# Optimization experiments

Hardware: AMD Instinct MI355X
Metric: run time of the kernel (lower is better)

Reference implementation:

```python
import jax, jax.numpy as jnp
import numpy as np

B, S, D = 2, 2048, 1024
N_QK, N_V, N_KNOW = 4096, 4096, 8192
N_HEADS = 16
MAX_K_QK, MAX_K_V, MAX_K_KNOW = 32, 32, 64
LN_EPS = 1e-6


def _unit_norm(key, shape, scale=1.0):
    x = jax.random.normal(key, shape, jnp.float32)
    return x / (jnp.linalg.norm(x, axis=-1, keepdims=True) + 1e-8) * scale


def setup_inputs() -> dict:
    key = jax.random.key(0)
    ks = jax.random.split(key, 12)
    return {
        "x": jax.random.normal(ks[0], (B, S, D), jnp.float32),
        "qk_emb": _unit_norm(ks[1], (N_QK, D)),
        "qk_w": _unit_norm(ks[2], (N_QK, D)),
        "v_emb": _unit_norm(ks[3], (N_V, D)),
        "v_w": _unit_norm(ks[4], (N_V, D)),
        "know_emb": _unit_norm(ks[5], (N_KNOW, D)),
        "know_w": _unit_norm(ks[6], (N_KNOW, D)),
        "tau_attn_k": jax.random.normal(ks[7], (D, 3), jnp.float32) * (1.0 / np.sqrt(D)),
        "tau_attn_b": jnp.zeros((3,), jnp.float32),
        "tau_know_k": jax.random.normal(ks[8], (D, 1), jnp.float32) * (1.0 / np.sqrt(D)),
        "tau_know_b": jnp.zeros((1,), jnp.float32),
        "expand_O": jax.random.normal(ks[9], (D, D), jnp.float32) * 0.02,
        "ln1_scale": jnp.ones((D,), jnp.float32),
        "ln1_bias": jnp.zeros((D,), jnp.float32),
        "ln2_scale": jnp.ones((D,), jnp.float32),
        "ln2_bias": jnp.zeros((D,), jnp.float32),
    }


def _layer_norm(x, scale, bias):
    mean = jnp.mean(x, axis=-1, keepdims=True)
    var = jnp.mean(jnp.square(x - mean), axis=-1, keepdims=True)
    return (x - mean) / jnp.sqrt(var + LN_EPS) * scale + bias


def threshold_gate(scores, tau, max_k):
    # scores: [B,S,N], tau: [B,S,1]
    raw = scores - tau
    gate = jnp.where(raw > 0, raw, 1e-8 * jnp.exp(raw))
    exp_gate = jnp.exp(gate) - 1.0
    topk_vals, _ = jax.lax.top_k(exp_gate, min(max_k, scores.shape[-1]))
    thr = topk_vals[:, :, -1:]
    exp_gate = jnp.where(exp_gate >= thr, exp_gate, 0.0)
    gate_sum = exp_gate.sum(axis=-1, keepdims=True) + 1e-8
    strength = jnp.tanh(exp_gate.max(axis=-1, keepdims=True))
    return exp_gate / gate_sum * strength


@jax.checkpoint
def sense_emit_full(x, emb, w, gate):
    # [B,S,D] @ [D,N] -> gated [B,S,N] -> [B,S,D]
    return ((x @ emb.T) * gate) @ w


def _block(x, qk_emb, qk_w, v_emb, v_w, know_emb, know_w,
           tau_attn_k, tau_attn_b, tau_know_k, tau_know_b,
           expand_O, ln1_scale, ln1_bias, ln2_scale, ln2_bias):
    # ---- attention circuit (deterministic; dropout = identity) ----
    normed = _layer_norm(x, ln1_scale, ln1_bias)
    scores_qk = normed @ qk_emb.T           # [B,S,N_QK]
    scores_v = normed @ v_emb.T             # [B,S,N_V]
    tau_all = normed @ tau_attn_k + tau_attn_b  # [B,S,3]
    g_Q = threshold_gate(scores_qk, tau_all[:, :, 0:1], MAX_K_QK)
    g_K = threshold_gate(scores_qk, tau_all[:, :, 1:2], MAX_K_QK)
    g_V = threshold_gate(scores_v, tau_all[:, :, 2:3], MAX_K_V)
    t_qk = 1.0 / qk_emb.shape[0]
    t_v = 1.0 / v_emb.shape[0]
    a_aux = (((g_Q.mean(axis=(0, 1)) - t_qk) ** 2).sum() * g_Q.shape[-1]
             + ((g_K.mean(axis=(0, 1)) - t_qk) ** 2).sum() * g_K.shape[-1]
             + ((g_V.mean(axis=(0, 1)) - t_v) ** 2).sum() * g_V.shape[-1])

    Q = sense_emit_full(normed, qk_emb, qk_w, g_Q)
    K = sense_emit_full(normed, qk_emb, qk_w, g_K)
    V = sense_emit_full(normed, v_emb, v_w, g_V)

    Bs, Ss, Ds = x.shape
    d_head = Ds // N_HEADS
    Q = Q.reshape(Bs, Ss, N_HEADS, d_head).transpose(0, 2, 1, 3)
    K = K.reshape(Bs, Ss, N_HEADS, d_head).transpose(0, 2, 1, 3)
    V = V.reshape(Bs, Ss, N_HEADS, d_head).transpose(0, 2, 1, 3)
    scale = jnp.sqrt(jnp.float32(d_head))
    attn = jnp.einsum('bhsd,bhtd->bhst', Q, K) / scale
    causal = jnp.tril(jnp.ones((Ss, Ss), dtype=jnp.bool_))
    attn = jnp.where(causal, attn, jnp.finfo(attn.dtype).min)
    attn = jax.nn.softmax(attn, axis=-1)
    out = jnp.einsum('bhst,bhtd->bhsd', attn, V)
    out = out.transpose(0, 2, 1, 3).reshape(Bs, Ss, Ds)
    out = out @ expand_O
    x = x + out

    # ---- knowledge circuit ----
    normed = _layer_norm(x, ln2_scale, ln2_bias)
    scores_k = normed @ know_emb.T          # [B,S,N_KNOW]
    tau_k = normed @ tau_know_k + tau_know_b
    gate = threshold_gate(scores_k, tau_k, MAX_K_KNOW)
    t_k = 1.0 / know_emb.shape[0]
    k_aux = ((gate.mean(axis=(0, 1)) - t_k) ** 2).sum() * know_emb.shape[0]
    know_out = sense_emit_full(normed, know_emb, know_w, gate)
    x = x + know_out
    return x, a_aux + k_aux


def reference(x, qk_emb, qk_w, v_emb, v_w, know_emb, know_w,
              tau_attn_k, tau_attn_b, tau_know_k, tau_know_b,
              expand_O, ln1_scale, ln1_bias, ln2_scale, ln2_bias):
    return _block(x, qk_emb, qk_w, v_emb, v_w, know_emb, know_w,
                  tau_attn_k, tau_attn_b, tau_know_k, tau_know_b,
                  expand_O, ln1_scale, ln1_bias, ln2_scale, ln2_bias)
```

## Files before the change

kernel.cpp:

```cpp
#include <hip/hip_runtime.h>

#define TOK   4096
#define DIM   1024
#define NQK   4096
#define NV    4096
#define NKN   8192
#define SLEN  2048
#define NH    16
#define DH    64
#define CAPA  48
#define CAPK  96
#define APAD  72

typedef float  f32x4  __attribute__((ext_vector_type(4)));
typedef short  short8 __attribute__((ext_vector_type(8)));
typedef unsigned int  u32;
typedef unsigned short u16;

__device__ __forceinline__ u16 f2bf(float f) {
    u32 u = __float_as_uint(f);
    u32 r = (u + 0x7fffu + ((u >> 16) & 1u)) >> 16;
    return (u16)r;
}
__device__ __forceinline__ float bf2f(u16 v) { return __uint_as_float(((u32)v) << 16); }

__device__ __forceinline__ u16 bfkey(u16 b) {
    return (b & 0x8000u) ? (u16)(~b) : (u16)(b | 0x8000u);
}
__device__ __forceinline__ u16 keybf(u16 k) {
    return (k & 0x8000u) ? (u16)(k & 0x7fffu) : (u16)(~k);
}

__device__ __forceinline__ f32x4 mfma_bf16(short8 a, short8 b, f32x4 c) {
    asm volatile("v_mfma_f32_16x16x32_bf16 %0, %1, %2, %0"
                 : "+v"(c) : "v"(a), "v"(b));
    return c;
}

__device__ __forceinline__ void gload16(const u16* g, u16* s) {
    __builtin_amdgcn_global_load_lds((const __attribute__((address_space(1))) void*)g,
                                     (__attribute__((address_space(3))) void*)s, 16, 0, 0);
}

__device__ __forceinline__ float blockReduceF(float v, float* red, int wave, int lane) {
#pragma unroll
    for (int off = 32; off > 0; off >>= 1) v += __shfl_xor(v, off);
    __syncthreads();
    if (lane == 0) red[wave] = v;
    __syncthreads();
    return red[0] + red[1] + red[2] + red[3];
}

__global__ __launch_bounds__(256) void k_convert_all(const float* __restrict__ p0,
                                                     const float* __restrict__ p1,
                                                     const float* __restrict__ p2,
                                                     const float* __restrict__ p3,
                                                     const float* __restrict__ p4,
                                                     const float* __restrict__ p5,
                                                     u16* __restrict__ o0, u16* __restrict__ o1,
                                                     u16* __restrict__ o2, u16* __restrict__ o3,
                                                     u16* __restrict__ o4, u16* __restrict__ o5) {
    const int S0 = 1048576, S1 = 2097152, S2 = 4194304, S3 = 5242880, S4 = 6291456, S5 = 8388608;
    for (int i = blockIdx.x * 256 + threadIdx.x; i < S5; i += gridDim.x * 256) {
        const float* in; u16* out; int off;
        if (i < S0)      { in = p0; out = o0; off = i; }
        else if (i < S1) { in = p1; out = o1; off = i - S0; }
        else if (i < S2) { in = p2; out = o2; off = i - S1; }
        else if (i < S3) { in = p3; out = o3; off = i - S2; }
        else if (i < S4) { in = p4; out = o4; off = i - S3; }
        else             { in = p5; out = o5; off = i - S4; }
        float4 v = reinterpret_cast<const float4*>(in)[off];
        reinterpret_cast<ushort4*>(out)[off] = make_ushort4(f2bf(v.x), f2bf(v.y), f2bf(v.z), f2bf(v.w));
    }
}

__global__ __launch_bounds__(256) void k_transpose_bf16(const float* __restrict__ in,
                                                        u16* __restrict__ out) {
    __shared__ float tile[32][33];
    int bx = blockIdx.x * 32;
    int by = blockIdx.y * 32;
    int tx = threadIdx.x & 31;
    int ty = threadIdx.x >> 5;
    for (int r = ty; r < 32; r += 8)
        tile[r][tx] = in[(size_t)(by + r) * DIM + bx + tx];
    __syncthreads();
    for (int r = ty; r < 32; r += 8)
        out[(size_t)(bx + r) * DIM + by + tx] = f2bf(tile[tx][r]);
}

__global__ __launch_bounds__(256) void k_ln_tau(const float* __restrict__ x,
                                                const float* __restrict__ sc,
                                                const float* __restrict__ bi,
                                                const float* __restrict__ tauk,
                                                const float* __restrict__ taub,
                                                int ntau,
                                                u16* __restrict__ nrm,
                                                float* __restrict__ tau_out) {
    __shared__ float red[4];
    int t = blockIdx.x, tid = threadIdx.x, wave = tid >> 6, lane = tid & 63;
    const float4 xv = reinterpret_cast<const float4*>(x + (size_t)t * DIM)[tid];
    float s = xv.x + xv.y + xv.z + xv.w;
    s = blockReduceF(s, red, wave, lane);
    float mean = s * (1.0f / DIM);
    float d0 = xv.x - mean, d1 = xv.y - mean, d2 = xv.z - mean, d3 = xv.w - mean;
    float ss = d0 * d0 + d1 * d1 + d2 * d2 + d3 * d3;
    ss = blockReduceF(ss, red, wave, lane);
    float rstd = rsqrtf(ss * (1.0f / DIM) + 1e-6f);
    const float4 scv = reinterpret_cast<const float4*>(sc)[tid];
    const float4 biv = reinterpret_cast<const float4*>(bi)[tid];
    float n0 = d0 * rstd * scv.x + biv.x;
    float n1 = d1 * rstd * scv.y + biv.y;
    float n2 = d2 * rstd * scv.z + biv.z;
    float n3 = d3 * rstd * scv.w + biv.w;
    ushort4 o = make_ushort4(f2bf(n0), f2bf(n1), f2bf(n2), f2bf(n3));
    reinterpret_cast<ushort4*>(nrm + (size_t)t * DIM)[tid] = o;
    int d = tid * 4;
    for (int j = 0; j < ntau; j++) {
        float p = n0 * tauk[(size_t)(d + 0) * ntau + j] + n1 * tauk[(size_t)(d + 1) * ntau + j]
                + n2 * tauk[(size_t)(d + 2) * ntau + j] + n3 * tauk[(size_t)(d + 3) * ntau + j];
        p = blockReduceF(p, red, wave, lane);
        if (tid == 0) tau_out[(size_t)t * ntau + j] = p + taub[j];
    }
}

template<int TAG, int KEYOUT>
__global__ __launch_bounds__(256) void k_gemm_bt(const u16* __restrict__ A,
                                                 const u16* __restrict__ B,
                                                 void* __restrict__ Cv,
                                                 int M, int N, int K,
                                                 const float* __restrict__ res) {
    __shared__ __align__(16) u16 As[3][4096];
    __shared__ __align__(16) u16 Bs[3][4096];
    int tid = threadIdx.x;
    int wave = tid >> 6, lane = tid & 63;
    int m0 = blockIdx.y * 128, n0 = blockIdx.x * 128;
    int wm = (wave >> 1) * 64, wn = (wave & 1) * 64;
    int kg = lane >> 4, l15 = lane & 15;

    const u16* gA0 = A + (size_t)(m0 + lane) * K + wave * 8;
    const u16* gA1 = A + (size_t)(m0 + 64 + lane) * K + wave * 8;
    const u16* gB0 = B + (size_t)(n0 + lane) * K + wave * 8;
    const u16* gB1 = B + (size_t)(n0 + 64 + lane) * K + wave * 8;

    f32x4 acc[4][4];
#pragma unroll
    for (int i = 0; i < 4; i++)
#pragma unroll
        for (int j = 0; j < 4; j++) { f32x4 z = {0.f, 0.f, 0.f, 0.f}; acc[i][j] = z; }

    const int nsteps = K >> 5;
#pragma unroll
    for (int p = 0; p < 2; p++) {
        int kk = p * 32;
        gload16(gA0 + kk, As[p] + wave * 1024);
        gload16(gA1 + kk, As[p] + wave * 1024 + 512);
        gload16(gB0 + kk, Bs[p] + wave * 1024);
        gload16(gB1 + kk, Bs[p] + wave * 1024 + 512);
    }

    int cur = 0, nxt = 2;
    for (int s = 0; s < nsteps; s++) {
        asm volatile("s_waitcnt vmcnt(4)" ::: "memory");
        __builtin_amdgcn_s_barrier();
        {
            int tn = (s + 2 < nsteps) ? s + 2 : nsteps - 1;
            int kn = tn * 32;
            gload16(gA0 + kn, As[nxt] + wave * 1024);
            gload16(gA1 + kn, As[nxt] + wave * 1024 + 512);
            gload16(gB0 + kn, Bs[nxt] + wave * 1024);
            gload16(gB1 + kn, Bs[nxt] + wave * 1024 + 512);
        }
        const u16* Ac = As[cur];
        const u16* Bc = Bs[cur];
        short8 af[4], bg[4];
#pragma unroll
        for (int mi = 0; mi < 4; mi++) {
            int row = wm + mi * 16 + l15;
            af[mi] = *reinterpret_cast<const short8*>(&Ac[(kg * 128 + row) * 8]);
        }
#pragma unroll
        for (int ni = 0; ni < 4; ni++) {
            int row = wn + ni * 16 + l15;
            bg[ni] = *reinterpret_cast<const short8*>(&Bc[(kg * 128 + row) * 8]);
        }
#pragma unroll
        for (int mi = 0; mi < 4; mi++)
#pragma unroll
            for (int ni = 0; ni < 4; ni++)
                acc[mi][ni] = mfma_bf16(af[mi], bg[ni], acc[mi][ni]);
        cur = (cur == 2) ? 0 : cur + 1;
        nxt = (nxt == 2) ? 0 : nxt + 1;
    }
    asm volatile("s_waitcnt vmcnt(0)" ::: "memory");
    asm volatile("s_nop 7\n\ts_nop 7");
#pragma unroll
    for (int mi = 0; mi < 4; mi++) {
#pragma unroll
        for (int ni = 0; ni < 4; ni++) {
            int col = n0 + wn + ni * 16 + l15;
#pragma unroll
            for (int r = 0; r < 4; r++) {
                int rowm = m0 + wm + mi * 16 + (lane >> 4) * 4 + r;
                size_t idx = (size_t)rowm * N + col;
                float v = acc[mi][ni][r];
                if (KEYOUT) {
                    ((u16*)Cv)[idx] = bfkey(f2bf(v));
                } else {
                    if (res) v += res[idx];
                    ((float*)Cv)[idx] = v;
                }
            }
        }
    }
}

template<int TWO, int RES>
__global__ __launch_bounds__(256) void k_gate_emit(const u16* __restrict__ keys_g, int NC, int ksel,
                                                   int row_off,
                                                   const float* __restrict__ tau, int tau_stride, int tcol0,
                                                   const u16* __restrict__ w,
                                                   u16* __restrict__ OA, u16* __restrict__ OB,
                                                   float* __restrict__ io,
                                                   float* __restrict__ csA, float* __restrict__ csB) {
    extern __shared__ u16 keys[];
    __shared__ int   hist[256];
    __shared__ int   scnt;
    __shared__ int   dsel;
    __shared__ int   knext;
    __shared__ int   sidx[CAPK];
    __shared__ float svA[CAPK];
    __shared__ float svB[CAPK];
    int r = blockIdx.x, tid = threadIdx.x, wave = tid >> 6, lane = tid & 63;
    int t = row_off + r;
    const int cap = TWO ? CAPA : (RES ? CAPK : CAPA);

    const uint4* srow8 = reinterpret_cast<const uint4*>(keys_g + (size_t)r * NC);
    for (int c = tid; c < NC / 8; c += 256)
        reinterpret_cast<uint4*>(keys)[c] = srow8[c];
    if (tid == 0) scnt = 0;

    u32 prefix = 0;
    int krem = ksel;
#pragma unroll
    for (int pass = 0; pass < 2; pass++) {
        int shift = 8 - pass * 8;
        hist[tid] = 0;
        __syncthreads();
        u32 pmask = (pass == 0) ? 0u : 0xFF00u;
        for (int i = tid; i < NC; i += 256) {
            u32 ky = keys[i];
            if ((ky & pmask) == prefix)
                atomicAdd(&hist[(ky >> shift) & 255], 1);
        }
        __syncthreads();
        int v = hist[tid];
#pragma unroll
        for (int off = 1; off < 256; off <<= 1) {
            int other = (tid + off < 256) ? hist[tid + off] : 0;
            __syncthreads();
            v += other;
            hist[tid] = v;
            __syncthreads();
        }
        int sfx = v;
        int sfx_next = (tid < 255) ? hist[tid + 1] : 0;
        if (sfx >= krem && (tid == 255 || sfx_next < krem)) {
            dsel = tid;
            knext = krem - sfx_next;
        }
        __syncthreads();
        prefix |= ((u32)dsel) << shift;
        krem = knext;
        __syncthreads();
    }
    u32 thr = prefix;

    for (int i = tid; i < NC; i += 256) {
        u32 ky = keys[i];
        if (ky >= thr) {
            int p = atomicAdd(&scnt, 1);
            if (p < cap) {
                sidx[p] = i;
                svA[p] = bf2f(keybf((u16)ky));
            }
        }
    }
    __syncthreads();
    int n = scnt < cap ? scnt : cap;

    if (wave == 0) {
        float tA = tau[(size_t)t * tau_stride + tcol0];
        float tB = TWO ? tau[(size_t)t * tau_stride + tcol0 + 1] : 0.f;
        float sumA = 0.f, mxA = -1e30f, sumB = 0.f, mxB = -1e30f;
        float sv0 = (lane < n) ? svA[lane] : 0.f;
        float sv1 = (lane + 64 < n) ? svA[lane + 64] : 0.f;
        for (int i = lane; i < n; i += 64) {
            float sv = svA[i];
            float rA = sv - tA;
            float gA = rA > 0.f ? rA : 1e-8f * expf(rA);
            float eA = expf(gA) - 1.0f;
            sumA += eA; mxA = fmaxf(mxA, eA);
            if (TWO) {
                float rB = sv - tB;
                float gB = rB > 0.f ? rB : 1e-8f * expf(rB);
                float eB = expf(gB) - 1.0f;
                sumB += eB; mxB = fmaxf(mxB, eB);
            }
        }
#pragma unroll
        for (int off = 32; off > 0; off >>= 1) {
            sumA += __shfl_xor(sumA, off); mxA = fmaxf(mxA, __shfl_xor(mxA, off));
            sumB += __shfl_xor(sumB, off); mxB = fmaxf(mxB, __shfl_xor(mxB, off));
        }
        float fA = tanhf(mxA) / (sumA + 1e-8f);
        float fB = tanhf(mxB) / (sumB + 1e-8f);
        if (lane < n) {
            float sv = sv0; int ci = sidx[lane];
            float rA = sv - tA;
            float gA = rA > 0.f ? rA : 1e-8f * expf(rA);
            float ga = (expf(gA) - 1.0f) * fA;
            svA[lane] = ga * sv;
            atomicAdd(&csA[ci], ga);
            if (TWO) {
                float rB = sv - tB;
                float gB = rB > 0.f ? rB : 1e-8f * expf(rB);
                float gb = (expf(gB) - 1.0f) * fB;
                svB[lane] = gb * sv;
                atomicAdd(&csB[ci], gb);
            }
        }
        if (lane + 64 < n) {
            float sv = sv1; int ci = sidx[lane + 64];
            float rA = sv - tA;
            float gA = rA > 0.f ? rA : 1e-8f * expf(rA);
            float ga = (expf(gA) - 1.0f) * fA;
            svA[lane + 64] = ga * sv;
            atomicAdd(&csA[ci], ga);
            if (TWO) {
                float rB = sv - tB;
                float gB = rB > 0.f ? rB : 1e-8f * expf(rB);
                float gb = (expf(gB) - 1.0f) * fB;
                svB[lane + 64] = gb * sv;
                atomicAdd(&csB[ci], gb);
            }
        }
    }
    __syncthreads();

    float a0 = 0, a1 = 0, a2 = 0, a3 = 0, b0 = 0, b1 = 0, b2 = 0, b3 = 0;
    float4 base;
    if (RES) base = reinterpret_cast<const float4*>(io + (size_t)t * DIM)[tid];
    int s = 0;
    for (; s + 4 <= n; s += 4) {
        const ushort4 w0 = reinterpret_cast<const ushort4*>(w + (size_t)sidx[s]     * DIM)[tid];
        const ushort4 w1 = reinterpret_cast<const ushort4*>(w + (size_t)sidx[s + 1] * DIM)[tid];
        const ushort4 w2 = reinterpret_cast<const ushort4*>(w + (size_t)sidx[s + 2] * DIM)[tid];
        const ushort4 w3 = reinterpret_cast<const ushort4*>(w + (size_t)sidx[s + 3] * DIM)[tid];
        float vA0 = svA[s], vA1 = svA[s + 1], vA2 = svA[s + 2], vA3 = svA[s + 3];
        a0 += vA0 * bf2f(w0.x) + vA1 * bf2f(w1.x) + vA2 * bf2f(w2.x) + vA3 * bf2f(w3.x);
        a1 += vA0 * bf2f(w0.y) + vA1 * bf2f(w1.y) + vA2 * bf2f(w2.y) + vA3 * bf2f(w3.y);
        a2 += vA0 * bf2f(w0.z) + vA1 * bf2f(w1.z) + vA2 * bf2f(w2.z) + vA3 * bf2f(w3.z);
        a3 += vA0 * bf2f(w0.w) + vA1 * bf2f(w1.w) + vA2 * bf2f(w2.w) + vA3 * bf2f(w3.w);
        if (TWO) {
            float vB0 = svB[s], vB1 = svB[s + 1], vB2 = svB[s + 2], vB3 = svB[s + 3];
            b0 += vB0 * bf2f(w0.x) + vB1 * bf2f(w1.x) + vB2 * bf2f(w2.x) + vB3 * bf2f(w3.x);
            b1 += vB0 * bf2f(w0.y) + vB1 * bf2f(w1.y) + vB2 * bf2f(w2.y) + vB3 * bf2f(w3.y);
            b2 += vB0 * bf2f(w0.z) + vB1 * bf2f(w1.z) + vB2 * bf2f(w2.z) + vB3 * bf2f(w3.z);
            b3 += vB0 * bf2f(w0.w) + vB1 * bf2f(w1.w) + vB2 * bf2f(w2.w) + vB3 * bf2f(w3.w);
        }
    }
    for (; s < n; s++) {
        const ushort4 wv = reinterpret_cast<const ushort4*>(w + (size_t)sidx[s] * DIM)[tid];
        float va = svA[s];
        a0 += va * bf2f(wv.x); a1 += va * bf2f(wv.y); a2 += va * bf2f(wv.z); a3 += va * bf2f(wv.w);
        if (TWO) {
            float vb = svB[s];
            b0 += vb * bf2f(wv.x); b1 += vb * bf2f(wv.y); b2 += vb * bf2f(wv.z); b3 += vb * bf2f(wv.w);
        }
    }
    if (RES) {
        reinterpret_cast<float4*>(io + (size_t)t * DIM)[tid] =
            make_float4(base.x + a0, base.y + a1, base.z + a2, base.w + a3);
    } else {
        reinterpret_cast<ushort4*>(OA + (size_t)t * DIM)[tid] = make_ushort4(f2bf(a0), f2bf(a1), f2bf(a2), f2bf(a3));
        if (TWO)
            reinterpret_cast<ushort4*>(OB + (size_t)t * DIM)[tid] = make_ushort4(f2bf(b0), f2bf(b1), f2bf(b2), f2bf(b3));
    }
}

__global__ __launch_bounds__(256) void k_attn(const u16* __restrict__ Q,
                                              const u16* __restrict__ K,
                                              const u16* __restrict__ V,
                                              u16* __restrict__ O) {
    __shared__ __align__(16) u16 Qs[64 * APAD];
    __shared__ __align__(16) u16 Ks[64 * APAD];
    __shared__ __align__(16) u16 Vt[64 * APAD];
    __shared__ __align__(16) u16 Ps[4][16 * APAD];
    int tid = threadIdx.x, wave = tid >> 6, lane = tid & 63;
    int h = blockIdx.x, bb = blockIdx.y, qt = blockIdx.z;
    int q0 = qt * 64;
    size_t base = ((size_t)bb * SLEN) * DIM + (size_t)h * DH;
    int sr = tid >> 2, sc = (tid & 3) * 16;
    int g = lane >> 4, l15 = lane & 15;

    {
        const u16* qp = Q + base + (size_t)(q0 + sr) * DIM + sc;
        *reinterpret_cast<short8*>(&Qs[sr * APAD + sc])     = *reinterpret_cast<const short8*>(qp);
        *reinterpret_cast<short8*>(&Qs[sr * APAD + sc + 8]) = *reinterpret_cast<const short8*>(qp + 8);
    }
    __syncthreads();
    short8 qa0 = *reinterpret_cast<const short8*>(&Qs[(wave * 16 + l15) * APAD + g * 8]);
    short8 qa1 = *reinterpret_cast<const short8*>(&Qs[(wave * 16 + l15) * APAD + 32 + g * 8]);

    float m[4], l[4];
    f32x4 oacc[4];
#pragma unroll
    for (int i = 0; i < 4; i++) {
        m[i] = -1e30f; l[i] = 0.f;
        f32x4 z = {0.f, 0.f, 0.f, 0.f}; oacc[i] = z;
    }
    u16* pw = &Ps[wave][0];

    for (int kc = 0; kc <= qt; kc++) {
        __syncthreads();
        {
            const u16* kp = K + base + (size_t)(kc * 64 + sr) * DIM + sc;
            *reinterpret_cast<short8*>(&Ks[sr * APAD + sc])     = *reinterpret_cast<const short8*>(kp);
            *reinterpret_cast<short8*>(&Ks[sr * APAD + sc + 8]) = *reinterpret_cast<const short8*>(kp + 8);
            const u16* vp = V + base + (size_t)(kc * 64 + sr) * DIM + sc;
            short8 w0 = *reinterpret_cast<const short8*>(vp);
            short8 w1 = *reinterpret_cast<const short8*>(vp + 8);
            const u16* w0p = reinterpret_cast<const u16*>(&w0);
            const u16* w1p = reinterpret_cast<const u16*>(&w1);
#pragma unroll
            for (int j = 0; j < 16; j++) {
                int d = sc + j;
                int phys = (((sr >> 3) + d + (d >> 4)) & 7);
                Vt[d * APAD + phys * 8 + (sr & 7)] = (j < 8) ? w0p[j] : w1p[j - 8];
            }
        }
        __syncthreads();

        f32x4 s4[4];
#pragma unroll
        for (int ks = 0; ks < 4; ks++) {
            f32x4 z = {0.f, 0.f, 0.f, 0.f}; s4[ks] = z;
            short8 kb0 = *reinterpret_cast<const short8*>(&Ks[(ks * 16 + l15) * APAD + g * 8]);
            short8 kb1 = *reinterpret_cast<const short8*>(&Ks[(ks * 16 + l15) * APAD + 32 + g * 8]);
            s4[ks] = mfma_bf16(qa0, kb0, s4[ks]);
            s4[ks] = mfma_bf16(qa1, kb1, s4[ks]);
        }
        asm volatile("s_nop 7\n\ts_nop 7");

        int key_base = kc * 64 + l15;
#pragma unroll
        for (int ks = 0; ks < 4; ks++) {
            int key = key_base + ks * 16;
#pragma unroll
            for (int r = 0; r < 4; r++) {
                int q_abs = q0 + wave * 16 + g * 4 + r;
                float sv = s4[ks][r] * 0.125f;
                s4[ks][r] = (key > q_abs) ? -1e30f : sv;
            }
        }

#pragma unroll
        for (int r = 0; r < 4; r++) {
            float mx = fmaxf(fmaxf(s4[0][r], s4[1][r]), fmaxf(s4[2][r], s4[3][r]));
            mx = fmaxf(mx, __shfl_xor(mx, 1));
            mx = fmaxf(mx, __shfl_xor(mx, 2));
            mx = fmaxf(mx, __shfl_xor(mx, 4));
            mx = fmaxf(mx, __shfl_xor(mx, 8));
            float mnew = fmaxf(m[r], mx);
            float al = __expf(m[r] - mnew);
            m[r] = mnew;
            float p0 = __expf(s4[0][r] - mnew);
            float p1 = __expf(s4[1][r] - mnew);
            float p2 = __expf(s4[2][r] - mnew);
            float p3 = __expf(s4[3][r] - mnew);
            float ps = p0 + p1 + p2 + p3;
            ps += __shfl_xor(ps, 1);
            ps += __shfl_xor(ps, 2);
            ps += __shfl_xor(ps, 4);
            ps += __shfl_xor(ps, 8);
            l[r] = l[r] * al + ps;
#pragma unroll
            for (int ds_ = 0; ds_ < 4; ds_++) oacc[ds_][r] *= al;
            int row = g * 4 + r;
            pw[row * APAD +  0 + l15] = f2bf(p0);
            pw[row * APAD + 16 + l15] = f2bf(p1);
            pw[row * APAD + 32 + l15] = f2bf(p2);
            pw[row * APAD + 48 + l15] = f2bf(p3);
        }

        short8 pa0 = *reinterpret_cast<const short8*>(&pw[l15 * APAD + g * 8]);
        short8 pa1 = *reinterpret_cast<const short8*>(&pw[l15 * APAD + 32 + g * 8]);
#pragma unroll
        for (int dsub = 0; dsub < 4; dsub++) {
            int d = dsub * 16 + l15;
            int rot = d + (d >> 4);
            short8 vb0 = *reinterpret_cast<const short8*>(&Vt[d * APAD + (((0 + g) + rot) & 7) * 8]);
            short8 vb1 = *reinterpret_cast<const short8*>(&Vt[d * APAD + (((4 + g) + rot) & 7) * 8]);
            oacc[dsub] = mfma_bf16(pa0, vb0, oacc[dsub]);
            oacc[dsub] = mfma_bf16(pa1, vb1, oacc[dsub]);
        }
    }
    asm volatile("s_nop 7\n\ts_nop 7");

#pragma unroll
    for (int r = 0; r < 4; r++) {
        float inv = 1.0f / l[r];
        int row = q0 + wave * 16 + g * 4 + r;
#pragma unroll
        for (int dsub = 0; dsub < 4; dsub++) {
            O[base + (size_t)row * DIM + dsub * 16 + l15] = f2bf(oacc[dsub][r] * inv);
        }
    }
}

__global__ __launch_bounds__(256) void k_aux(const float* __restrict__ cs,
                                             float* __restrict__ out_aux) {
    __shared__ float red[4];
    int gtid = blockIdx.x * 256 + threadIdx.x;
    float acc = 0.f;
    for (int i = gtid; i < 3 * 4096 + 8192; i += gridDim.x * 256) {
        float mean = cs[i] * (1.0f / 4096.0f);
        float tN, Nf;
        if (i < 12288) { tN = 1.0f / 4096.0f; Nf = 4096.0f; }
        else           { tN = 1.0f / 8192.0f; Nf = 8192.0f; }
        float d = mean - tN;
        acc += d * d * Nf;
    }
    acc = blockReduceF(acc, red, threadIdx.x >> 6, threadIdx.x & 63);
    if (threadIdx.x == 0) atomicAdd(out_aux, acc);
}

extern "C" void kernel_launch(void* const* d_in, const int* in_sizes, int n_in,
                              void* d_out, int out_size, void* d_ws, size_t ws_size,
                              hipStream_t stream) {
    const float* x         = (const float*)d_in[0];
    const float* qk_emb    = (const float*)d_in[1];
    const float* qk_w      = (const float*)d_in[2];
    const float* v_emb     = (const float*)d_in[3];
    const float* v_w       = (const float*)d_in[4];
    const float* know_emb  = (const float*)d_in[5];
    const float* know_w    = (const float*)d_in[6];
    const float* tau_attn_k = (const float*)d_in[7];
    const float* tau_attn_b = (const float*)d_in[8];
    const float* tau_know_k = (const float*)d_in[9];
    const float* tau_know_b = (const float*)d_in[10];
    const float* expand_O  = (const float*)d_in[11];
    const float* ln1_s     = (const float*)d_in[12];
    const float* ln1_b     = (const float*)d_in[13];
    const float* ln2_s     = (const float*)d_in[14];
    const float* ln2_b     = (const float*)d_in[15];
    float* out = (float*)d_out;
    char*  ws  = (char*)d_ws;

    u16*   nrm_bf   = (u16*)(ws + 0);
    u16*   qkemb_bf = (u16*)(ws + 8388608);
    u16*   vemb_bf  = (u16*)(ws + 16777216);
    u16*   knemb_bf = (u16*)(ws + 25165824);
    u16*   expT_bf  = (u16*)(ws + 41943040);
    u16*   attn_bf  = (u16*)(ws + 44040192);
    u16*   qkw_bf   = (u16*)(ws + 52428800);
    u16*   vw_bf    = (u16*)(ws + 60817408);
    u16*   knw_bf   = (u16*)(ws + 69206016);
    u16*   Qb       = (u16*)(ws + 85983232);
    u16*   Kb       = (u16*)(ws + 94371840);
    u16*   Vb       = (u16*)(ws + 102760448);
    u16*   keysbuf  = (u16*)(ws + 111149056);
    float* tauA     = (float*)(ws + 185384960);
    float* tauKn    = (float*)(ws + 185434112);
    float* colsum   = (float*)(ws + 185450496);
    const size_t WS_NEEDED = 185532416;
    if (ws_size < WS_NEEDED) return;

    float* colQ = colsum, *colK = colsum + 4096, *colV = colsum + 8192, *colKn = colsum + 12288;

    hipMemsetAsync(colsum, 0, 20480 * sizeof(float), stream);
    hipMemsetAsync(out + (size_t)TOK * DIM, 0, sizeof(float), stream);

    k_convert_all<<<2048, 256, 0, stream>>>(qk_emb, v_emb, know_emb, qk_w, v_w, know_w,
                                            qkemb_bf, vemb_bf, knemb_bf, qkw_bf, vw_bf, knw_bf);
    k_transpose_bf16<<<dim3(32, 32), 256, 0, stream>>>(expand_O, expT_bf);

    k_ln_tau<<<TOK, 256, 0, stream>>>(x, ln1_s, ln1_b, tau_attn_k, tau_attn_b, 3, nrm_bf, tauA);

    k_gemm_bt<0, 1><<<dim3(NQK / 128, TOK / 128), 256, 0, stream>>>(nrm_bf, qkemb_bf, keysbuf, TOK, NQK, DIM, nullptr);
    k_gate_emit<1, 0><<<TOK, 256, NQK * sizeof(u16), stream>>>(keysbuf, NQK, 32, 0, tauA, 3, 0,
                                                               qkw_bf, Qb, Kb, nullptr, colQ, colK);
    k_gemm_bt<1, 1><<<dim3(NV / 128, TOK / 128), 256, 0, stream>>>(nrm_bf, vemb_bf, keysbuf, TOK, NV, DIM, nullptr);
    k_gate_emit<0, 0><<<TOK, 256, NV * sizeof(u16), stream>>>(keysbuf, NV, 32, 0, tauA, 3, 2,
                                                              vw_bf, Vb, nullptr, nullptr, colV, nullptr);

    k_attn<<<dim3(NH, 2, SLEN / 64), 256, 0, stream>>>(Qb, Kb, Vb, attn_bf);

    k_gemm_bt<2, 0><<<dim3(DIM / 128, TOK / 128), 256, 0, stream>>>(attn_bf, expT_bf, out, TOK, DIM, DIM, x);

    k_ln_tau<<<TOK, 256, 0, stream>>>(out, ln2_s, ln2_b, tau_know_k, tau_know_b, 1, nrm_bf, tauKn);

    k_gemm_bt<3, 1><<<dim3(NKN / 128, TOK / 128), 256, 0, stream>>>(nrm_bf, knemb_bf, keysbuf, TOK, NKN, DIM, nullptr);
    k_gate_emit<0, 1><<<TOK, 256, NKN * sizeof(u16), stream>>>(keysbuf, NKN, 64, 0, tauKn, 1, 0,
                                                               knw_bf, nullptr, nullptr, out, colKn, nullptr);

    k_aux<<<20, 256, 0, stream>>>(colsum, out + (size_t)TOK * DIM);
}
```

Baseline: 742.5 us.

## Merge QK and V score GEMMs, double-buffer GEMM LDS, load Q directly

The QK and V score GEMMs become one launch with N=8192. It writes both halves into a shared keys buffer, and the gate kernel now takes a separate row stride (ldk) so each half can be read from it. This assumes the bf16 V embedding sits directly after the QK embedding in the workspace. The GEMM mainloop drops from three LDS stages to two and adds a second barrier, so the prefetch of tile s+2 can safely overwrite the buffer just consumed. This cuts LDS use, which may raise occupancy, at the cost of extra synchronisation. The attention kernel loads Q fragments straight from global memory into registers, removing the Q shared-memory tile and one block barrier.

```diff
diff --git a/kernel.cpp b/kernel.cpp
--- a/kernel.cpp
+++ b/kernel.cpp
@@ -129,8 +129,8 @@
                                                  void* __restrict__ Cv,
                                                  int M, int N, int K,
                                                  const float* __restrict__ res) {
-    __shared__ __align__(16) u16 As[3][4096];
-    __shared__ __align__(16) u16 Bs[3][4096];
+    __shared__ __align__(16) u16 As[2][4096];
+    __shared__ __align__(16) u16 Bs[2][4096];
     int tid = threadIdx.x;
     int wave = tid >> 6, lane = tid & 63;
     int m0 = blockIdx.y * 128, n0 = blockIdx.x * 128;
@@ -158,38 +158,39 @@
         gload16(gB1 + kk, Bs[p] + wave * 1024 + 512);
     }
 
-    int cur = 0, nxt = 2;
     for (int s = 0; s < nsteps; s++) {
+        int cur = s & 1;
         asm volatile("s_waitcnt vmcnt(4)" ::: "memory");
         __builtin_amdgcn_s_barrier();
+        __builtin_amdgcn_sched_barrier(0);
+        const u16* Ac = As[cur];
+        const u16* Bc = Bs[cur];
+        short8 af[4], bg[4];
+#pragma unroll
+        for (int mi = 0; mi < 4; mi++) {
+            int row = wm + mi * 16 + l15;
+            af[mi] = *reinterpret_cast<const short8*>(&Ac[(kg * 128 + row) * 8]);
+        }
+#pragma unroll
+        for (int ni = 0; ni < 4; ni++) {
+            int row = wn + ni * 16 + l15;
+            bg[ni] = *reinterpret_cast<const short8*>(&Bc[(kg * 128 + row) * 8]);
+        }
+#pragma unroll
+        for (int mi = 0; mi < 4; mi++)
+#pragma unroll
+            for (int ni = 0; ni < 4; ni++)
+                acc[mi][ni] = mfma_bf16(af[mi], bg[ni], acc[mi][ni]);
+        __builtin_amdgcn_s_barrier();
+        __builtin_amdgcn_sched_barrier(0);
         {
             int tn = (s + 2 < nsteps) ? s + 2 : nsteps - 1;
             int kn = tn * 32;
-            gload16(gA0 + kn, As[nxt] + wave * 1024);
-            gload16(gA1 + kn, As[nxt] + wave * 1024 + 512);
-            gload16(gB0 + kn, Bs[nxt] + wave * 1024);
-            gload16(gB1 + kn, Bs[nxt] + wave * 1024 + 512);
-        }
-        const u16* Ac = As[cur];
-        const u16* Bc = Bs[cur];
-        short8 af[4], bg[4];
-#pragma unroll
-        for (int mi = 0; mi < 4; mi++) {
-            int row = wm + mi * 16 + l15;
-            af[mi] = *reinterpret_cast<const short8*>(&Ac[(kg * 128 + row) * 8]);
-        }
-#pragma unroll
-        for (int ni = 0; ni < 4; ni++) {
-            int row = wn + ni * 16 + l15;
-            bg[ni] = *reinterpret_cast<const short8*>(&Bc[(kg * 128 + row) * 8]);
-        }
-#pragma unroll
-        for (int mi = 0; mi < 4; mi++)
-#pragma unroll
-            for (int ni = 0; ni < 4; ni++)
-                acc[mi][ni] = mfma_bf16(af[mi], bg[ni], acc[mi][ni]);
-        cur = (cur == 2) ? 0 : cur + 1;
-        nxt = (nxt == 2) ? 0 : nxt + 1;
+            gload16(gA0 + kn, As[cur] + wave * 1024);
+            gload16(gA1 + kn, As[cur] + wave * 1024 + 512);
+            gload16(gB0 + kn, Bs[cur] + wave * 1024);
+            gload16(gB1 + kn, Bs[cur] + wave * 1024 + 512);
+        }
     }
     asm volatile("s_waitcnt vmcnt(0)" ::: "memory");
     asm volatile("s_nop 7\n\ts_nop 7");
@@ -215,8 +216,8 @@
 }
 
 template<int TWO, int RES>
-__global__ __launch_bounds__(256) void k_gate_emit(const u16* __restrict__ keys_g, int NC, int ksel,
-                                                   int row_off,
+__global__ __launch_bounds__(256) void k_gate_emit(const u16* __restrict__ keys_g, int ldk,
+                                                   int NC, int ksel, int row_off,
                                                    const float* __restrict__ tau, int tau_stride, int tcol0,
                                                    const u16* __restrict__ w,
                                                    u16* __restrict__ OA, u16* __restrict__ OB,
@@ -234,7 +235,7 @@
     int t = row_off + r;
     const int cap = TWO ? CAPA : (RES ? CAPK : CAPA);
 
-    const uint4* srow8 = reinterpret_cast<const uint4*>(keys_g + (size_t)r * NC);
+    const uint4* srow8 = reinterpret_cast<const uint4*>(keys_g + (size_t)r * ldk);
     for (int c = tid; c < NC / 8; c += 256)
         reinterpret_cast<uint4*>(keys)[c] = srow8[c];
     if (tid == 0) scnt = 0;
@@ -392,7 +393,6 @@
                                               const u16* __restrict__ K,
                                               const u16* __restrict__ V,
                                               u16* __restrict__ O) {
-    __shared__ __align__(16) u16 Qs[64 * APAD];
     __shared__ __align__(16) u16 Ks[64 * APAD];
     __shared__ __align__(16) u16 Vt[64 * APAD];
     __shared__ __align__(16) u16 Ps[4][16 * APAD];
@@ -403,14 +403,9 @@
     int sr = tid >> 2, sc = (tid & 3) * 16;
     int g = lane >> 4, l15 = lane & 15;
 
-    {
-        const u16* qp = Q + base + (size_t)(q0 + sr) * DIM + sc;
-        *reinterpret_cast<short8*>(&Qs[sr * APAD + sc])     = *reinterpret_cast<const short8*>(qp);
-        *reinterpret_cast<short8*>(&Qs[sr * APAD + sc + 8]) = *reinterpret_cast<const short8*>(qp + 8);
-    }
-    __syncthreads();
-    short8 qa0 = *reinterpret_cast<const short8*>(&Qs[(wave * 16 + l15) * APAD + g * 8]);
-    short8 qa1 = *reinterpret_cast<const short8*>(&Qs[(wave * 16 + l15) * APAD + 32 + g * 8]);
+    const u16* qrow = Q + base + (size_t)(q0 + wave * 16 + l15) * DIM;
+    short8 qa0 = *reinterpret_cast<const short8*>(qrow + g * 8);
+    short8 qa1 = *reinterpret_cast<const short8*>(qrow + 32 + g * 8);
 
     float m[4], l[4];
     f32x4 oacc[4];
@@ -587,11 +582,10 @@
 
     k_ln_tau<<<TOK, 256, 0, stream>>>(x, ln1_s, ln1_b, tau_attn_k, tau_attn_b, 3, nrm_bf, tauA);
 
-    k_gemm_bt<0, 1><<<dim3(NQK / 128, TOK / 128), 256, 0, stream>>>(nrm_bf, qkemb_bf, keysbuf, TOK, NQK, DIM, nullptr);
-    k_gate_emit<1, 0><<<TOK, 256, NQK * sizeof(u16), stream>>>(keysbuf, NQK, 32, 0, tauA, 3, 0,
+    k_gemm_bt<0, 1><<<dim3(8192 / 128, TOK / 128), 256, 0, stream>>>(nrm_bf, qkemb_bf, keysbuf, TOK, 8192, DIM, nullptr);
+    k_gate_emit<1, 0><<<TOK, 256, NQK * sizeof(u16), stream>>>(keysbuf, 8192, NQK, 32, 0, tauA, 3, 0,
                                                                qkw_bf, Qb, Kb, nullptr, colQ, colK);
-    k_gemm_bt<1, 1><<<dim3(NV / 128, TOK / 128), 256, 0, stream>>>(nrm_bf, vemb_bf, keysbuf, TOK, NV, DIM, nullptr);
-    k_gate_emit<0, 0><<<TOK, 256, NV * sizeof(u16), stream>>>(keysbuf, NV, 32, 0, tauA, 3, 2,
+    k_gate_emit<0, 0><<<TOK, 256, NV * sizeof(u16), stream>>>(keysbuf + 4096, 8192, NV, 32, 0, tauA, 3, 2,
                                                               vw_bf, Vb, nullptr, nullptr, colV, nullptr);
 
     k_attn<<<dim3(NH, 2, SLEN / 64), 256, 0, stream>>>(Qb, Kb, Vb, attn_bf);
@@ -601,7 +595,7 @@
     k_ln_tau<<<TOK, 256, 0, stream>>>(out, ln2_s, ln2_b, tau_know_k, tau_know_b, 1, nrm_bf, tauKn);
 
     k_gemm_bt<3, 1><<<dim3(NKN / 128, TOK / 128), 256, 0, stream>>>(nrm_bf, knemb_bf, keysbuf, TOK, NKN, DIM, nullptr);
-    k_gate_emit<0, 1><<<TOK, 256, NKN * sizeof(u16), stream>>>(keysbuf, NKN, 64, 0, tauKn, 1, 0,
+    k_gate_emit<0, 1><<<TOK, 256, NKN * sizeof(u16), stream>>>(keysbuf, NKN, NKN, 64, 0, tauKn, 1, 0,
                                                                knw_bf, nullptr, nullptr, out, colKn, nullptr);
 
     k_aux<<<20, 256, 0, stream>>>(colsum, out + (size_t)TOK * DIM);
```

Result: faster. 726.3 us (-2.2%).
